# Optimization experiments

Measured on AMD Instinct MI355X. Metric: run time of the kernel, lower is better.

Reference implementation:

```python
import jax, jax.numpy as jnp
import numpy as np

NUM_CLASSES = 80
BATCH_PER_IMG = 512
FG_CAP = 128  # int(512 * 0.25)
IOU_THRESH = 0.5
STRIDE = 16.0
OUT = 7
RATIO = 2


def _pairwise_iou(gt, pr):
    # gt: [M,4], pr: [N,4] in (x1,y1,x2,y2) -> [M,N]
    area_g = (gt[:, 2] - gt[:, 0]) * (gt[:, 3] - gt[:, 1])
    area_p = (pr[:, 2] - pr[:, 0]) * (pr[:, 3] - pr[:, 1])
    lt = jnp.maximum(gt[:, None, :2], pr[None, :, :2])
    rb = jnp.minimum(gt[:, None, 2:], pr[None, :, 2:])
    wh = jnp.clip(rb - lt, 0.0)
    inter = wh[..., 0] * wh[..., 1]
    union = area_g[:, None] + area_p[None, :] - inter
    return jnp.where(inter > 0, inter / union, 0.0)


def _match_and_sample(iou, gt_cls, rand):
    # iou: [M,N]; Matcher(thresholds=[0.5], labels=[0,1], no low-quality)
    matched_vals = iou.max(axis=0)
    matched_idxs = iou.argmax(axis=0)
    matched = matched_vals >= IOU_THRESH
    cls = jnp.where(matched, gt_cls[matched_idxs], NUM_CLASSES)
    fg = cls != NUM_CLASSES
    bg = ~fg

    def _rank(mask):
        # rank of each masked element under random permutation (rand in [0,1))
        key = jnp.where(mask, rand, 2.0)
        return jnp.argsort(jnp.argsort(key))

    num_fg = jnp.minimum(fg.sum(), FG_CAP)
    sel_fg = fg & (_rank(fg) < num_fg)
    num_bg = jnp.minimum(BATCH_PER_IMG - num_fg, bg.sum())
    sel_bg = bg & (_rank(bg) < num_bg)
    score = sel_fg * 2.0 + sel_bg * 1.0
    _, sampled = jax.lax.top_k(score, BATCH_PER_IMG)
    return sampled, cls[sampled], matched_idxs[sampled]


def _roi_align(feat, rois, batch_idx):
    # feat: [B,C,H,W], rois: [R,4] image coords, aligned=True ROIAlignV2
    B, C, H, W = feat.shape
    f = feat.transpose(0, 2, 3, 1)  # [B,H,W,C]
    b = rois / STRIDE - 0.5
    x1, y1, x2, y2 = b[:, 0], b[:, 1], b[:, 2], b[:, 3]
    g = (jnp.arange(OUT * RATIO, dtype=feat.dtype) + 0.5) / RATIO  # [14] in bin units
    xs = x1[:, None] + g[None, :] * ((x2 - x1) / OUT)[:, None]  # [R,14]
    ys = y1[:, None] + g[None, :] * ((y2 - y1) / OUT)[:, None]
    xs = jnp.clip(xs, 0.0, W - 1)
    ys = jnp.clip(ys, 0.0, H - 1)
    x0 = jnp.floor(xs).astype(jnp.int32)
    y0 = jnp.floor(ys).astype(jnp.int32)
    x1i = jnp.minimum(x0 + 1, W - 1)
    y1i = jnp.minimum(y0 + 1, H - 1)
    lx = xs - x0.astype(xs.dtype)
    ly = ys - y0.astype(ys.dtype)
    bb = batch_idx[:, None, None]
    v00 = f[bb, y0[:, :, None], x0[:, None, :]]  # [R,14,14,C]
    v01 = f[bb, y0[:, :, None], x1i[:, None, :]]
    v10 = f[bb, y1i[:, :, None], x0[:, None, :]]
    v11 = f[bb, y1i[:, :, None], x1i[:, None, :]]
    wy1 = ly[:, :, None, None]
    wy0 = 1.0 - wy1
    wx1 = lx[:, None, :, None]
    wx0 = 1.0 - wx1
    val = v00 * wy0 * wx0 + v01 * wy0 * wx1 + v10 * wy1 * wx0 + v11 * wy1 * wx1
    R = rois.shape[0]
    pooled = val.reshape(R, OUT, RATIO, OUT, RATIO, C).mean(axis=(2, 4))  # [R,7,7,C]
    return pooled.transpose(0, 3, 1, 2).reshape(R, -1)  # channel-major flatten, matches torch


def setup_inputs() -> dict:
    key = jax.random.key(0)
    ks = jax.random.split(key, 14)
    B, N, M, C, H, W = 2, 2000, 64, 256, 64, 64
    IMG = 1024.0

    def mk_boxes(k, b, n):
        pts = jax.random.uniform(k, (b, n, 2, 2), jnp.float32) * (IMG - 16.0)
        lo = pts.min(axis=2)
        hi = pts.max(axis=2) + 8.0
        return jnp.concatenate([lo, hi], axis=-1)

    D = C * OUT * OUT  # 12544
    FC = 1024
    return {
        "features": jax.random.normal(ks[0], (B, C, H, W), jnp.float32),
        "proposal_boxes": mk_boxes(ks[1], B, N),
        "gt_boxes": mk_boxes(ks[2], B, M),
        "gt_classes": jax.random.randint(ks[3], (B, M), 0, NUM_CLASSES),
        "rand_scores": jax.random.uniform(ks[4], (B, N + M), jnp.float32),
        "fc1_w": jax.random.normal(ks[5], (D, FC), jnp.float32) * 0.02,
        "fc1_b": jnp.zeros((FC,), jnp.float32),
        "fc2_w": jax.random.normal(ks[6], (FC, FC), jnp.float32) * 0.02,
        "fc2_b": jnp.zeros((FC,), jnp.float32),
        "cls_w": jax.random.normal(ks[7], (FC, NUM_CLASSES + 1), jnp.float32) * 0.02,
        "cls_b": jnp.zeros((NUM_CLASSES + 1,), jnp.float32),
        "box_w": jax.random.normal(ks[8], (FC, NUM_CLASSES * 4), jnp.float32) * 0.02,
        "box_b": jnp.zeros((NUM_CLASSES * 4,), jnp.float32),
    }


def reference(features, proposal_boxes, gt_boxes, gt_classes, rand_scores,
              fc1_w, fc1_b, fc2_w, fc2_b, cls_w, cls_b, box_w, box_b):
    # proposal_append_gt: concat GT boxes onto proposals
    all_boxes = jnp.concatenate([proposal_boxes, gt_boxes], axis=1)  # [B,N+M,4]
    iou = jax.vmap(_pairwise_iou)(gt_boxes, all_boxes)  # [B,M,N+M]
    sampled, cls, _ = jax.vmap(_match_and_sample)(iou, gt_classes, rand_scores)
    rois = jnp.take_along_axis(all_boxes, sampled[..., None], axis=1).reshape(-1, 4)
    B = features.shape[0]
    bidx = jnp.repeat(jnp.arange(B), BATCH_PER_IMG)
    x = _roi_align(features, rois, bidx)  # [R, 12544]
    x = jax.nn.relu(x @ fc1_w + fc1_b)
    x = jax.nn.relu(x @ fc2_w + fc2_b)
    out = jnp.concatenate([x @ cls_w + cls_b, x @ box_w + box_b], axis=-1)  # [R, 401]
    return out
```

## Files before the change

kernel.cpp:

```cpp
#include <hip/hip_runtime.h>
#include <cstdint>
#include <cstddef>

constexpr int B_   = 2;
constexpr int N_   = 2000;
constexpr int M_   = 64;
constexpr int NB_  = N_ + M_;
constexpr int C_   = 256;
constexpr int H_   = 64;
constexpr int W_   = 64;
constexpr int RPI  = 512;
constexpr int RTOT = B_ * RPI;
constexpr int FG_CAP_ = 128;
constexpr int D_   = C_ * 49;
constexpr int FC_  = 1024;
constexpr int OUTC = 401;
constexpr int KT1  = D_ / 32;
constexpr int KT2  = FC_ / 32;
constexpr float IOU_T = 0.5f;

typedef _Float16 f16;
typedef f16   f16x8 __attribute__((ext_vector_type(8)));
typedef float f32x4 __attribute__((ext_vector_type(4)));

__device__ __forceinline__ void tile_load16(const void* g, void* l) {
  __builtin_amdgcn_global_load_lds(
      (const __attribute__((address_space(1))) unsigned int*)g,
      (__attribute__((address_space(3))) unsigned int*)l, 16, 0, 0);
}

__global__ __launch_bounds__(256) void k_transpose(const float* __restrict__ in,
                                                   float* __restrict__ out) {
  __shared__ float tile[32][33];
  int b = blockIdx.z, hw0 = blockIdx.x * 32, c0 = blockIdx.y * 32;
  int tx = threadIdx.x, ty = threadIdx.y;
#pragma unroll
  for (int i = ty; i < 32; i += 8)
    tile[i][tx] = in[((size_t)b * C_ + c0 + i) * (H_ * W_) + hw0 + tx];
  __syncthreads();
#pragma unroll
  for (int i = ty; i < 32; i += 8)
    out[((size_t)b * (H_ * W_) + hw0 + i) * C_ + c0 + tx] = tile[tx][i];
}

__global__ __launch_bounds__(1024) void k_iou(const float* __restrict__ prop,
                                              const float* __restrict__ gt,
                                              unsigned char* __restrict__ fg,
                                              int* __restrict__ cnt) {
  __shared__ float s_gt[M_ * 4];
  __shared__ float s_area[M_];
  __shared__ int s_cnt;
  int b = blockIdx.x, t = threadIdx.x;
  if (t == 0) s_cnt = 0;
  if (t < M_ * 4) s_gt[t] = gt[(size_t)b * M_ * 4 + t];
  __syncthreads();
  if (t < M_) {
    float x1 = s_gt[t*4], y1 = s_gt[t*4+1], x2 = s_gt[t*4+2], y2 = s_gt[t*4+3];
    s_area[t] = (x2 - x1) * (y2 - y1);
  }
  __syncthreads();
  int local = 0;
  for (int j = t; j < NB_; j += 1024) {
    float bx1, by1, bx2, by2;
    if (j < N_) {
      const float* p = prop + ((size_t)b * N_ + j) * 4;
      bx1 = p[0]; by1 = p[1]; bx2 = p[2]; by2 = p[3];
    } else {
      const float* p = s_gt + (j - N_) * 4;
      bx1 = p[0]; by1 = p[1]; bx2 = p[2]; by2 = p[3];
    }
    float area_p = (bx2 - bx1) * (by2 - by1);
    float best = 0.f;
    for (int g = 0; g < M_; ++g) {
      float lx = fmaxf(s_gt[g*4], bx1),   lyv = fmaxf(s_gt[g*4+1], by1);
      float rx = fminf(s_gt[g*4+2], bx2), ry  = fminf(s_gt[g*4+3], by2);
      float w = fmaxf(rx - lx, 0.f), h = fmaxf(ry - lyv, 0.f);
      float inter = w * h;
      float iou = inter > 0.f ? inter / (s_area[g] + area_p - inter) : 0.f;
      best = fmaxf(best, iou);
    }
    int f = (best >= IOU_T) ? 1 : 0;
    fg[(size_t)b * NB_ + j] = (unsigned char)f;
    local += f;
  }
  atomicAdd(&s_cnt, local);
  __syncthreads();
  if (t == 0) cnt[b] = s_cnt;
}

__global__ __launch_bounds__(256) void k_rank(const float* __restrict__ rnd,
                                              const unsigned char* __restrict__ fg,
                                              const int* __restrict__ cnt,
                                              unsigned char* __restrict__ sel) {
  __shared__ unsigned long long s_key[NB_];
  int b = blockIdx.y, t = threadIdx.x;
  for (int j = t; j < NB_; j += 256) {
    float r = rnd[(size_t)b * NB_ + j];
    int f = (int)fg[(size_t)b * NB_ + j];
    float ck = r + 2.0f * (float)f;
    unsigned int ib = __float_as_uint(ck);
    s_key[j] = ((unsigned long long)ib << 11) | (unsigned int)j;
  }
  __syncthreads();
  int j = blockIdx.x * 256 + t;
  int jj = (j < NB_) ? j : 0;
  unsigned long long uj = s_key[jj];
  int rank_all = 0;
  const uint4* kp = (const uint4*)s_key;
#pragma unroll 4
  for (int k2 = 0; k2 < NB_ / 2; ++k2) {
    uint4 v = kp[k2];
    unsigned long long k0 = ((unsigned long long)v.y << 32) | v.x;
    unsigned long long k1 = ((unsigned long long)v.w << 32) | v.z;
    rank_all += (k0 < uj) ? 1 : 0;
    rank_all += (k1 < uj) ? 1 : 0;
  }
  if (j >= NB_) return;
  int fgcnt  = cnt[b];
  int num_fg = min(fgcnt, FG_CAP_);
  int num_bg = min(RPI - num_fg, NB_ - fgcnt);
  int myfg   = (uj >> 11) >= 0x40000000ull ? 1 : 0;
  int rank   = rank_all - (myfg ? (NB_ - fgcnt) : 0);
  int lim    = myfg ? num_fg : num_bg;
  sel[(size_t)b * NB_ + j] =
      (rank < lim) ? (unsigned char)(myfg ? 2 : 1) : (unsigned char)0;
}

__global__ __launch_bounds__(64) void k_place(const float* __restrict__ prop,
                                              const float* __restrict__ gt,
                                              const int* __restrict__ cnt,
                                              const unsigned char* __restrict__ sel,
                                              float* __restrict__ rois) {
  int b = blockIdx.x, L = threadIdx.x;
  int fgcnt  = cnt[b];
  int num_fg = min(fgcnt, FG_CAP_);
  int num_bg = min(RPI - num_fg, NB_ - fgcnt);
  int S = num_fg + num_bg;
  int t2 = 0, t1 = 0, t0 = 0;
  unsigned long long lt = (L == 0) ? 0ull : ((~0ull) >> (64 - L));
  for (int c = 0; c < (NB_ + 63) / 64; ++c) {
    int j = c * 64 + L;
    int s = (j < NB_) ? (int)sel[(size_t)b * NB_ + j] : -1;
    unsigned long long m2 = __ballot(s == 2);
    unsigned long long m1 = __ballot(s == 1);
    unsigned long long m0 = __ballot(s == 0);
    int pos = -1;
    if (s == 2) {
      pos = t2 + __popcll(m2 & lt);
    } else if (s == 1) {
      pos = num_fg + t1 + __popcll(m1 & lt);
    } else if (s == 0) {
      int p0 = t0 + __popcll(m0 & lt);
      if (S + p0 < RPI) pos = S + p0;
    }
    if (pos >= 0) {
      const float* p = (j < N_) ? (prop + ((size_t)b * N_ + j) * 4)
                                : (gt + ((size_t)b * M_ + (j - N_)) * 4);
      float* o = rois + ((size_t)b * RPI + pos) * 4;
      o[0] = p[0]; o[1] = p[1]; o[2] = p[2]; o[3] = p[3];
    }
    t2 += __popcll(m2); t1 += __popcll(m1); t0 += __popcll(m0);
  }
}

__global__ __launch_bounds__(256) void k_roialign(const float* __restrict__ fT,
                                                  const float* __restrict__ rois,
                                                  f16* __restrict__ Ahi) {
  __shared__ float sv[8][257];
  int bin = blockIdx.x, mt = blockIdx.y;
  int c = threadIdx.x;
  int by = bin / 7, bx = bin % 7;
  for (int pass = 0; pass < 2; ++pass) {
    for (int r8 = 0; r8 < 8; ++r8) {
      int r = mt * 16 + pass * 8 + r8;
      const float* rp = rois + (size_t)r * 4;
      float x1 = rp[0] * 0.0625f - 0.5f;
      float y1 = rp[1] * 0.0625f - 0.5f;
      float x2 = rp[2] * 0.0625f - 0.5f;
      float y2 = rp[3] * 0.0625f - 0.5f;
      float stx = (x2 - x1) * (1.0f / 7.0f);
      float sty = (y2 - y1) * (1.0f / 7.0f);
      const float* fb = fT + (size_t)(r >> 9) * H_ * W_ * C_;
      float acc = 0.f;
#pragma unroll
      for (int s = 0; s < 4; ++s) {
        int oy = s >> 1, ox = s & 1;
        float xs = x1 + ((float)(2 * bx + ox) + 0.5f) * 0.5f * stx;
        float ys = y1 + ((float)(2 * by + oy) + 0.5f) * 0.5f * sty;
        xs = fminf(fmaxf(xs, 0.f), (float)(W_ - 1));
        ys = fminf(fmaxf(ys, 0.f), (float)(H_ - 1));
        int x0 = (int)floorf(xs), y0 = (int)floorf(ys);
        int x1i = min(x0 + 1, W_ - 1), y1i = min(y0 + 1, H_ - 1);
        float lx = xs - (float)x0, ly = ys - (float)y0;
        float v00 = fb[((size_t)y0 * W_ + x0) * C_ + c];
        float v01 = fb[((size_t)y0 * W_ + x1i) * C_ + c];
        float v10 = fb[((size_t)y1i * W_ + x0) * C_ + c];
        float v11 = fb[((size_t)y1i * W_ + x1i) * C_ + c];
        acc += v00*(1.f-ly)*(1.f-lx) + v01*(1.f-ly)*lx + v10*ly*(1.f-lx) + v11*ly*lx;
      }
      sv[r8][c] = acc * 0.25f;
    }
    __syncthreads();
    int kt   = c >> 5;
    int l5   = c & 31;
    int quad = l5 >> 3;
    int r8   = l5 & 7;
    int lane = quad * 16 + pass * 8 + r8;
    int cbase = kt * 32 + quad * 8;
    f16x8 hv;
#pragma unroll
    for (int jj = 0; jj < 8; ++jj) hv[jj] = (f16)sv[r8][cbase + jj];
    size_t off = ((size_t)(mt * KT1 + bin * 8 + kt) * 64 + lane) * 8;
    *(f16x8*)(Ahi + off) = hv;
    __syncthreads();
  }
}

__global__ __launch_bounds__(256) void k_convw(const float* __restrict__ src,
                                               const float* __restrict__ src2,
                                               f16* __restrict__ dst,
                                               int KTtot, int mode) {
  __shared__ float tile[32][65];
  int kt = blockIdx.x, ng = blockIdx.y;
  int t = threadIdx.x;
  int n0 = ng * 64;
  int col = t & 63;
#pragma unroll
  for (int p = 0; p < 8; ++p) {
    int r = p * 4 + (t >> 6);
    int k = kt * 32 + r;
    float v;
    if (mode == 0) {
      v = src[(size_t)k * 1024 + n0 + col];
    } else if (mode == 1) {
      int row = (k & 255) * 49 + (k >> 8);
      v = src[(size_t)row * 1024 + n0 + col];
    } else {
      int n = n0 + col;
      v = (n < 81) ? src[(size_t)k * 81 + n]
                   : ((n < 401) ? src2[(size_t)k * 320 + (n - 81)] : 0.f);
    }
    tile[r][col] = v;
  }
  __syncthreads();
  int sub = t >> 6, lane = t & 63;
  int nt = ng * 4 + sub;
  int nl = lane & 15, kg = lane >> 4;
  f16x8 h;
#pragma unroll
  for (int e = 0; e < 8; ++e)
    h[e] = (f16)tile[kg * 8 + e][sub * 16 + nl];
  *(f16x8*)(dst + ((size_t)(nt * KTtot + kt) * 64 + lane) * 8) = h;
}

__global__ __launch_bounds__(256, 2) void k_gemm_mfma(
    const f16* __restrict__ Ahi, const f16* __restrict__ Bw,
    float* __restrict__ P, int N, int KTtot, int ktPerSplit) {
  __shared__ f16 sAh[8 * 512];
  __shared__ f16 sB[8 * 512];
  int tid = threadIdx.x;
  int lane = tid & 63, w = tid >> 6;
  int wm = w >> 1, wn = w & 1;
  int bm = blockIdx.x, bn = blockIdx.y, z = blockIdx.z;
  int kt0 = z * ktPerSplit, ktEnd = kt0 + ktPerSplit;

  f32x4 acc[4][4];
#pragma unroll
  for (int i = 0; i < 4; ++i)
#pragma unroll
    for (int j = 0; j < 4; ++j) {
      f32x4 zv = {0.f, 0.f, 0.f, 0.f};
      acc[i][j] = zv;
    }

  for (int kt = kt0; kt < ktEnd; ++kt) {
#pragma unroll
    for (int tt = 0; tt < 4; ++tt) {
      int t = 4 * w + tt;
      const f16* g;
      f16* l;
      if (t < 8) { g = Ahi + ((size_t)(bm*8 + t)     * KTtot + kt) * 512; l = sAh + t * 512; }
      else       { g = Bw  + ((size_t)(bn*8 + (t-8)) * KTtot + kt) * 512; l = sB + (t-8) * 512; }
      tile_load16(g + lane * 8, l);
    }
    __syncthreads();
    f16x8 ah[4], bw[4];
#pragma unroll
    for (int i = 0; i < 4; ++i) {
      ah[i] = *(const f16x8*)(sAh + (wm*4 + i) * 512 + lane * 8);
      bw[i] = *(const f16x8*)(sB  + (wn*4 + i) * 512 + lane * 8);
    }
#pragma unroll
    for (int i = 0; i < 4; ++i)
#pragma unroll
      for (int j = 0; j < 4; ++j)
        acc[i][j] = __builtin_amdgcn_mfma_f32_16x16x32_f16(ah[i], bw[j], acc[i][j], 0, 0, 0);
    __syncthreads();
  }

  int quad = lane >> 4, cl = lane & 15;
  float* Pz = P + (size_t)z * 1024 * (size_t)N;
#pragma unroll
  for (int i = 0; i < 4; ++i) {
    int row = bm * 128 + wm * 64 + i * 16 + quad * 4;
#pragma unroll
    for (int j = 0; j < 4; ++j) {
      int col = bn * 128 + wn * 64 + j * 16 + cl;
#pragma unroll
      for (int r = 0; r < 4; ++r)
        Pz[(size_t)(row + r) * N + col] = acc[i][j][r];
    }
  }
}

__global__ __launch_bounds__(256) void k_combine(const float* __restrict__ P,
                                                 const float* __restrict__ bias,
                                                 f16* __restrict__ Ahi,
                                                 int nsplit) {
  int q = blockIdx.x * 256 + threadIdx.x;
  int lane = q & 63, tile = q >> 6;
  int mt = tile >> 5, kt = tile & 31;
  int m  = mt * 16 + (lane & 15);
  int n0 = kt * 32 + (lane >> 4) * 8;
  float v[8];
#pragma unroll
  for (int jj = 0; jj < 8; ++jj) v[jj] = bias[n0 + jj];
  for (int s = 0; s < nsplit; ++s) {
    const float* p = P + (size_t)s * 1048576 + (size_t)m * 1024 + n0;
#pragma unroll
    for (int jj = 0; jj < 8; ++jj) v[jj] += p[jj];
  }
  f16x8 hv;
#pragma unroll
  for (int jj = 0; jj < 8; ++jj) hv[jj] = (f16)fmaxf(v[jj], 0.f);
  *(f16x8*)(Ahi + (size_t)q * 8) = hv;
}

__global__ __launch_bounds__(256) void k_out(const float* __restrict__ P,
                                             const float* __restrict__ cls_b,
                                             const float* __restrict__ box_b,
                                             float* __restrict__ out, int nsplit) {
  int idx = blockIdx.x * 256 + threadIdx.x;
  if (idx >= RTOT * OUTC) return;
  int m = idx / OUTC, n = idx - m * OUTC;
  float v = (n < 81) ? cls_b[n] : box_b[n - 81];
  for (int s = 0; s < nsplit; ++s)
    v += P[(size_t)s * (1024 * 512) + (size_t)m * 512 + n];
  out[idx] = v;
}

extern "C" void kernel_launch(void* const* d_in, const int* in_sizes, int n_in,
                              void* d_out, int out_size, void* d_ws, size_t ws_size,
                              hipStream_t stream) {
  const float* features = (const float*)d_in[0];
  const float* prop     = (const float*)d_in[1];
  const float* gt       = (const float*)d_in[2];
  const float* rnd      = (const float*)d_in[4];
  const float* fc1_w    = (const float*)d_in[5];
  const float* fc1_b    = (const float*)d_in[6];
  const float* fc2_w    = (const float*)d_in[7];
  const float* fc2_b    = (const float*)d_in[8];
  const float* cls_w    = (const float*)d_in[9];
  const float* cls_b    = (const float*)d_in[10];
  const float* box_w    = (const float*)d_in[11];
  const float* box_b    = (const float*)d_in[12];
  float* out = (float*)d_out;

  char* base = (char*)d_ws;
  float* fT   = (float*)(base + 0);
  float* rois = (float*)(base + 8388608);
  char*  p2   = base + 8404992;
  f16* A1hi = (f16*)(base + 8404992);
  f16* W1   = (f16*)(base + 34095104);
  float* P1 = (float*)(base + 59785216);
  int s1 = (ws_size >= (size_t)59785216 + 8ull * 4194304) ? 8 : 4;
  f16* A2hi = (f16*)(p2 + 0);
  f16* W2   = (f16*)(p2 + 2097152);
  f16* A3hi = (f16*)(p2 + 4194304);
  f16* W3   = (f16*)(p2 + 6291456);
  float* P2 = (float*)(p2 + 7340032);
  float* P3 = (float*)(p2 + 24117248);
  unsigned char* g_fg  = (unsigned char*)(base + 59785216);
  unsigned char* g_sel = (unsigned char*)(base + 59785216 + 4160);
  int*           g_cnt = (int*)(base + 59785216 + 8320);

  k_transpose<<<dim3(128, 8, B_), dim3(32, 8), 0, stream>>>(features, fT);
  k_iou<<<dim3(B_), dim3(1024), 0, stream>>>(prop, gt, g_fg, g_cnt);
  k_rank<<<dim3((NB_ + 255) / 256, B_), dim3(256), 0, stream>>>(rnd, g_fg, g_cnt, g_sel);
  k_place<<<dim3(B_), dim3(64), 0, stream>>>(prop, gt, g_cnt, g_sel, rois);
  k_roialign<<<dim3(49, 64), dim3(256), 0, stream>>>(fT, rois, A1hi);
  k_convw<<<dim3(KT1, 16), dim3(256), 0, stream>>>(fc1_w, nullptr, W1, KT1, 1);
  k_gemm_mfma<<<dim3(8, 8, s1), dim3(256), 0, stream>>>(A1hi, W1, P1,
                                                        1024, KT1, KT1 / s1);
  k_combine<<<dim3(512), dim3(256), 0, stream>>>(P1, fc1_b, A2hi, s1);
  k_convw<<<dim3(KT2, 16), dim3(256), 0, stream>>>(fc2_w, nullptr, W2, KT2, 0);
  k_gemm_mfma<<<dim3(8, 8, 4), dim3(256), 0, stream>>>(A2hi, W2, P2,
                                                       1024, KT2, KT2 / 4);
  k_combine<<<dim3(512), dim3(256), 0, stream>>>(P2, fc2_b, A3hi, 4);
  k_convw<<<dim3(KT2, 8), dim3(256), 0, stream>>>(cls_w, box_w, W3, KT2, 2);
  k_gemm_mfma<<<dim3(8, 4, 4), dim3(256), 0, stream>>>(A3hi, W3, P3,
                                                       512, KT2, KT2 / 4);
  k_out<<<dim3((RTOT * OUTC + 255) / 256), dim3(256), 0, stream>>>(
      P3, cls_b, box_b, out, 4);
}
```

Measured before the change: 351.6 us.

## Merge front-end and weight-conversion kernels; store transposed features as fp16

Merges the feature transpose, fc1 weight conversion and IoU matching into one multi-role launch. Each combine step is merged with the next layer's weight conversion in the same way. The transposed feature map is now stored in fp16 instead of fp32, which halves the bytes written by the transpose and read by ROIAlign gathers. This cuts launch count and serial gaps between small kernels, at the cost of lower precision in the feature values used for bilinear interpolation.

```diff
diff --git a/kernel.cpp b/kernel.cpp
--- a/kernel.cpp
+++ b/kernel.cpp
@@ -29,63 +29,89 @@
       (__attribute__((address_space(3))) unsigned int*)l, 16, 0, 0);
 }
 
-__global__ __launch_bounds__(256) void k_transpose(const float* __restrict__ in,
-                                                   float* __restrict__ out) {
-  __shared__ float tile[32][33];
-  int b = blockIdx.z, hw0 = blockIdx.x * 32, c0 = blockIdx.y * 32;
-  int tx = threadIdx.x, ty = threadIdx.y;
-#pragma unroll
-  for (int i = ty; i < 32; i += 8)
-    tile[i][tx] = in[((size_t)b * C_ + c0 + i) * (H_ * W_) + hw0 + tx];
-  __syncthreads();
-#pragma unroll
-  for (int i = ty; i < 32; i += 8)
-    out[((size_t)b * (H_ * W_) + hw0 + i) * C_ + c0 + tx] = tile[tx][i];
-}
-
-__global__ __launch_bounds__(1024) void k_iou(const float* __restrict__ prop,
-                                              const float* __restrict__ gt,
-                                              unsigned char* __restrict__ fg,
-                                              int* __restrict__ cnt) {
-  __shared__ float s_gt[M_ * 4];
-  __shared__ float s_area[M_];
-  __shared__ int s_cnt;
-  int b = blockIdx.x, t = threadIdx.x;
-  if (t == 0) s_cnt = 0;
-  if (t < M_ * 4) s_gt[t] = gt[(size_t)b * M_ * 4 + t];
-  __syncthreads();
-  if (t < M_) {
-    float x1 = s_gt[t*4], y1 = s_gt[t*4+1], x2 = s_gt[t*4+2], y2 = s_gt[t*4+3];
-    s_area[t] = (x2 - x1) * (y2 - y1);
-  }
-  __syncthreads();
-  int local = 0;
-  for (int j = t; j < NB_; j += 1024) {
-    float bx1, by1, bx2, by2;
-    if (j < N_) {
-      const float* p = prop + ((size_t)b * N_ + j) * 4;
-      bx1 = p[0]; by1 = p[1]; bx2 = p[2]; by2 = p[3];
-    } else {
-      const float* p = s_gt + (j - N_) * 4;
-      bx1 = p[0]; by1 = p[1]; bx2 = p[2]; by2 = p[3];
-    }
-    float area_p = (bx2 - bx1) * (by2 - by1);
-    float best = 0.f;
-    for (int g = 0; g < M_; ++g) {
-      float lx = fmaxf(s_gt[g*4], bx1),   lyv = fmaxf(s_gt[g*4+1], by1);
-      float rx = fminf(s_gt[g*4+2], bx2), ry  = fminf(s_gt[g*4+3], by2);
-      float w = fmaxf(rx - lx, 0.f), h = fmaxf(ry - lyv, 0.f);
-      float inter = w * h;
-      float iou = inter > 0.f ? inter / (s_area[g] + area_p - inter) : 0.f;
-      best = fmaxf(best, iou);
-    }
-    int f = (best >= IOU_T) ? 1 : 0;
-    fg[(size_t)b * NB_ + j] = (unsigned char)f;
-    local += f;
-  }
-  atomicAdd(&s_cnt, local);
-  __syncthreads();
-  if (t == 0) cnt[b] = s_cnt;
+__global__ __launch_bounds__(256) void k_front(
+    const float* __restrict__ feat, const float* __restrict__ fc1w,
+    const float* __restrict__ prop, const float* __restrict__ gtb,
+    f16* __restrict__ fT, f16* __restrict__ W1,
+    unsigned char* __restrict__ fg, int* __restrict__ cnt) {
+  __shared__ __align__(16) char smem[8448];
+  int bid = blockIdx.x;
+  int t = threadIdx.x;
+  if (bid < 2048) {
+    float (*tile)[33] = (float(*)[33])smem;
+    int b = bid >> 10, rem = bid & 1023;
+    int hw0 = (rem & 127) * 32, c0 = (rem >> 7) * 32;
+    int tx = t & 31, ty = t >> 5;
+#pragma unroll
+    for (int i = ty; i < 32; i += 8)
+      tile[i][tx] = feat[((size_t)b * C_ + c0 + i) * (H_ * W_) + hw0 + tx];
+    __syncthreads();
+#pragma unroll
+    for (int i = ty; i < 32; i += 8)
+      fT[((size_t)b * (H_ * W_) + hw0 + i) * C_ + c0 + tx] = (f16)tile[tx][i];
+  } else if (bid < 2048 + 6272) {
+    float (*tile)[65] = (float(*)[65])smem;
+    int cb = bid - 2048;
+    int kt = cb % KT1, ng = cb / KT1;
+    int n0 = ng * 64;
+    int col = t & 63;
+#pragma unroll
+    for (int p = 0; p < 8; ++p) {
+      int r = p * 4 + (t >> 6);
+      int k = kt * 32 + r;
+      int row = (k & 255) * 49 + (k >> 8);
+      tile[r][col] = fc1w[(size_t)row * 1024 + n0 + col];
+    }
+    __syncthreads();
+    int sub = t >> 6, lane = t & 63;
+    int nt = ng * 4 + sub;
+    int nl = lane & 15, kg = lane >> 4;
+    f16x8 h;
+#pragma unroll
+    for (int e = 0; e < 8; ++e)
+      h[e] = (f16)tile[kg * 8 + e][sub * 16 + nl];
+    *(f16x8*)(W1 + ((size_t)(nt * KT1 + kt) * 64 + lane) * 8) = h;
+  } else {
+    float* s_gt = (float*)smem;
+    float* s_area = (float*)(smem + 1024);
+    int* s_cnt = (int*)(smem + 1280);
+    int b = bid - (2048 + 6272);
+    if (t == 0) *s_cnt = 0;
+    s_gt[t] = gtb[(size_t)b * M_ * 4 + t];
+    __syncthreads();
+    if (t < M_) {
+      float x1 = s_gt[t*4], y1 = s_gt[t*4+1], x2 = s_gt[t*4+2], y2 = s_gt[t*4+3];
+      s_area[t] = (x2 - x1) * (y2 - y1);
+    }
+    __syncthreads();
+    int local = 0;
+    for (int j = t; j < NB_; j += 256) {
+      float bx1, by1, bx2, by2;
+      if (j < N_) {
+        const float* p = prop + ((size_t)b * N_ + j) * 4;
+        bx1 = p[0]; by1 = p[1]; bx2 = p[2]; by2 = p[3];
+      } else {
+        const float* p = s_gt + (j - N_) * 4;
+        bx1 = p[0]; by1 = p[1]; bx2 = p[2]; by2 = p[3];
+      }
+      float area_p = (bx2 - bx1) * (by2 - by1);
+      float best = 0.f;
+      for (int g = 0; g < M_; ++g) {
+        float lx = fmaxf(s_gt[g*4], bx1),   lyv = fmaxf(s_gt[g*4+1], by1);
+        float rx = fminf(s_gt[g*4+2], bx2), ry  = fminf(s_gt[g*4+3], by2);
+        float w = fmaxf(rx - lx, 0.f), h = fmaxf(ry - lyv, 0.f);
+        float inter = w * h;
+        float iou = inter > 0.f ? inter / (s_area[g] + area_p - inter) : 0.f;
+        best = fmaxf(best, iou);
+      }
+      int f = (best >= IOU_T) ? 1 : 0;
+      fg[(size_t)b * NB_ + j] = (unsigned char)f;
+      local += f;
+    }
+    atomicAdd(s_cnt, local);
+    __syncthreads();
+    if (t == 0) cnt[b] = *s_cnt;
+  }
 }
 
 __global__ __launch_bounds__(256) void k_rank(const float* __restrict__ rnd,
@@ -163,7 +189,7 @@
   }
 }
 
-__global__ __launch_bounds__(256) void k_roialign(const float* __restrict__ fT,
+__global__ __launch_bounds__(256) void k_roialign(const f16* __restrict__ fT,
                                                   const float* __restrict__ rois,
                                                   f16* __restrict__ Ahi) {
   __shared__ float sv[8][257];
@@ -180,7 +206,7 @@
       float y2 = rp[3] * 0.0625f - 0.5f;
       float stx = (x2 - x1) * (1.0f / 7.0f);
       float sty = (y2 - y1) * (1.0f / 7.0f);
-      const float* fb = fT + (size_t)(r >> 9) * H_ * W_ * C_;
+      const f16* fb = fT + (size_t)(r >> 9) * H_ * W_ * C_;
       float acc = 0.f;
 #pragma unroll
       for (int s = 0; s < 4; ++s) {
@@ -192,10 +218,10 @@
         int x0 = (int)floorf(xs), y0 = (int)floorf(ys);
         int x1i = min(x0 + 1, W_ - 1), y1i = min(y0 + 1, H_ - 1);
         float lx = xs - (float)x0, ly = ys - (float)y0;
-        float v00 = fb[((size_t)y0 * W_ + x0) * C_ + c];
-        float v01 = fb[((size_t)y0 * W_ + x1i) * C_ + c];
-        float v10 = fb[((size_t)y1i * W_ + x0) * C_ + c];
-        float v11 = fb[((size_t)y1i * W_ + x1i) * C_ + c];
+        float v00 = (float)fb[((size_t)y0 * W_ + x0) * C_ + c];
+        float v01 = (float)fb[((size_t)y0 * W_ + x1i) * C_ + c];
+        float v10 = (float)fb[((size_t)y1i * W_ + x0) * C_ + c];
+        float v11 = (float)fb[((size_t)y1i * W_ + x1i) * C_ + c];
         acc += v00*(1.f-ly)*(1.f-lx) + v01*(1.f-ly)*lx + v10*ly*(1.f-lx) + v11*ly*lx;
       }
       sv[r8][c] = acc * 0.25f;
@@ -214,43 +240,6 @@
     *(f16x8*)(Ahi + off) = hv;
     __syncthreads();
   }
-}
-
-__global__ __launch_bounds__(256) void k_convw(const float* __restrict__ src,
-                                               const float* __restrict__ src2,
-                                               f16* __restrict__ dst,
-                                               int KTtot, int mode) {
-  __shared__ float tile[32][65];
-  int kt = blockIdx.x, ng = blockIdx.y;
-  int t = threadIdx.x;
-  int n0 = ng * 64;
-  int col = t & 63;
-#pragma unroll
-  for (int p = 0; p < 8; ++p) {
-    int r = p * 4 + (t >> 6);
-    int k = kt * 32 + r;
-    float v;
-    if (mode == 0) {
-      v = src[(size_t)k * 1024 + n0 + col];
-    } else if (mode == 1) {
-      int row = (k & 255) * 49 + (k >> 8);
-      v = src[(size_t)row * 1024 + n0 + col];
-    } else {
-      int n = n0 + col;
-      v = (n < 81) ? src[(size_t)k * 81 + n]
-                   : ((n < 401) ? src2[(size_t)k * 320 + (n - 81)] : 0.f);
-    }
-    tile[r][col] = v;
-  }
-  __syncthreads();
-  int sub = t >> 6, lane = t & 63;
-  int nt = ng * 4 + sub;
-  int nl = lane & 15, kg = lane >> 4;
-  f16x8 h;
-#pragma unroll
-  for (int e = 0; e < 8; ++e)
-    h[e] = (f16)tile[kg * 8 + e][sub * 16 + nl];
-  *(f16x8*)(dst + ((size_t)(nt * KTtot + kt) * 64 + lane) * 8) = h;
 }
 
 __global__ __launch_bounds__(256, 2) void k_gemm_mfma(
@@ -313,27 +302,61 @@
   }
 }
 
-__global__ __launch_bounds__(256) void k_combine(const float* __restrict__ P,
-                                                 const float* __restrict__ bias,
-                                                 f16* __restrict__ Ahi,
-                                                 int nsplit) {
-  int q = blockIdx.x * 256 + threadIdx.x;
-  int lane = q & 63, tile = q >> 6;
-  int mt = tile >> 5, kt = tile & 31;
-  int m  = mt * 16 + (lane & 15);
-  int n0 = kt * 32 + (lane >> 4) * 8;
-  float v[8];
-#pragma unroll
-  for (int jj = 0; jj < 8; ++jj) v[jj] = bias[n0 + jj];
-  for (int s = 0; s < nsplit; ++s) {
-    const float* p = P + (size_t)s * 1048576 + (size_t)m * 1024 + n0;
-#pragma unroll
-    for (int jj = 0; jj < 8; ++jj) v[jj] += p[jj];
-  }
-  f16x8 hv;
-#pragma unroll
-  for (int jj = 0; jj < 8; ++jj) hv[jj] = (f16)fmaxf(v[jj], 0.f);
-  *(f16x8*)(Ahi + (size_t)q * 8) = hv;
+__global__ __launch_bounds__(256) void k_mid(
+    const float* __restrict__ P, const float* __restrict__ bias,
+    f16* __restrict__ Adst, int nsplit,
+    const float* __restrict__ wsrc, const float* __restrict__ wsrc2,
+    f16* __restrict__ Wdst, int wmode) {
+  __shared__ float tile[32][65];
+  int bid = blockIdx.x;
+  int t = threadIdx.x;
+  if (bid < 512) {
+    int q = bid * 256 + t;
+    int lane = q & 63, tl = q >> 6;
+    int mt = tl >> 5, kt = tl & 31;
+    int m  = mt * 16 + (lane & 15);
+    int n0 = kt * 32 + (lane >> 4) * 8;
+    float v[8];
+#pragma unroll
+    for (int jj = 0; jj < 8; ++jj) v[jj] = bias[n0 + jj];
+    for (int s = 0; s < nsplit; ++s) {
+      const float* p = P + (size_t)s * 1048576 + (size_t)m * 1024 + n0;
+#pragma unroll
+      for (int jj = 0; jj < 8; ++jj) v[jj] += p[jj];
+    }
+    f16x8 hv;
+#pragma unroll
+    for (int jj = 0; jj < 8; ++jj) hv[jj] = (f16)fmaxf(v[jj], 0.f);
+    *(f16x8*)(Adst + (size_t)q * 8) = hv;
+  } else {
+    int cb = bid - 512;
+    int kt = cb & 31, ng = cb >> 5;
+    int n0 = ng * 64;
+    int col = t & 63;
+#pragma unroll
+    for (int p = 0; p < 8; ++p) {
+      int r = p * 4 + (t >> 6);
+      int k = kt * 32 + r;
+      float v;
+      if (wmode == 0) {
+        v = wsrc[(size_t)k * 1024 + n0 + col];
+      } else {
+        int n = n0 + col;
+        v = (n < 81) ? wsrc[(size_t)k * 81 + n]
+                     : ((n < 401) ? wsrc2[(size_t)k * 320 + (n - 81)] : 0.f);
+      }
+      tile[r][col] = v;
+    }
+    __syncthreads();
+    int sub = t >> 6, lane = t & 63;
+    int nt = ng * 4 + sub;
+    int nl = lane & 15, kg = lane >> 4;
+    f16x8 h;
+#pragma unroll
+    for (int e = 0; e < 8; ++e)
+      h[e] = (f16)tile[kg * 8 + e][sub * 16 + nl];
+    *(f16x8*)(Wdst + ((size_t)(nt * 32 + kt) * 64 + lane) * 8) = h;
+  }
 }
 
 __global__ __launch_bounds__(256) void k_out(const float* __restrict__ P,
@@ -367,7 +390,7 @@
   float* out = (float*)d_out;
 
   char* base = (char*)d_ws;
-  float* fT   = (float*)(base + 0);
+  f16*   fT   = (f16*)(base + 0);
   float* rois = (float*)(base + 8388608);
   char*  p2   = base + 8404992;
   f16* A1hi = (f16*)(base + 8404992);
@@ -384,20 +407,19 @@
   unsigned char* g_sel = (unsigned char*)(base + 59785216 + 4160);
   int*           g_cnt = (int*)(base + 59785216 + 8320);
 
-  k_transpose<<<dim3(128, 8, B_), dim3(32, 8), 0, stream>>>(features, fT);
-  k_iou<<<dim3(B_), dim3(1024), 0, stream>>>(prop, gt, g_fg, g_cnt);
+  k_front<<<dim3(2048 + 6272 + 2), dim3(256), 0, stream>>>(
+      features, fc1_w, prop, gt, fT, W1, g_fg, g_cnt);
   k_rank<<<dim3((NB_ + 255) / 256, B_), dim3(256), 0, stream>>>(rnd, g_fg, g_cnt, g_sel);
   k_place<<<dim3(B_), dim3(64), 0, stream>>>(prop, gt, g_cnt, g_sel, rois);
   k_roialign<<<dim3(49, 64), dim3(256), 0, stream>>>(fT, rois, A1hi);
-  k_convw<<<dim3(KT1, 16), dim3(256), 0, stream>>>(fc1_w, nullptr, W1, KT1, 1);
   k_gemm_mfma<<<dim3(8, 8, s1), dim3(256), 0, stream>>>(A1hi, W1, P1,
                                                         1024, KT1, KT1 / s1);
-  k_combine<<<dim3(512), dim3(256), 0, stream>>>(P1, fc1_b, A2hi, s1);
-  k_convw<<<dim3(KT2, 16), dim3(256), 0, stream>>>(fc2_w, nullptr, W2, KT2, 0);
+  k_mid<<<dim3(1024), dim3(256), 0, stream>>>(P1, fc1_b, A2hi, s1,
+                                              fc2_w, nullptr, W2, 0);
   k_gemm_mfma<<<dim3(8, 8, 4), dim3(256), 0, stream>>>(A2hi, W2, P2,
                                                        1024, KT2, KT2 / 4);
-  k_combine<<<dim3(512), dim3(256), 0, stream>>>(P2, fc2_b, A3hi, 4);
-  k_convw<<<dim3(KT2, 8), dim3(256), 0, stream>>>(cls_w, box_w, W3, KT2, 2);
+  k_mid<<<dim3(768), dim3(256), 0, stream>>>(P2, fc2_b, A3hi, 4,
+                                             cls_w, box_w, W3, 2);
   k_gemm_mfma<<<dim3(8, 4, 4), dim3(256), 0, stream>>>(A3hi, W3, P3,
                                                        512, KT2, KT2 / 4);
   k_out<<<dim3((RTOT * OUTC + 255) / 256), dim3(256), 0, stream>>>(
```

After: 398.8 us. 1.13x slower.
